# Optimization experiments

Hardware: AMD Instinct MI355X
Metric: run time of the kernel (lower is better)

## Reference

```python
import jax, jax.numpy as jnp
from jax import lax
import numpy as np

B, T, D, UNITS, NCLASSES = 256, 256, 512, 1024, 512


def setup_inputs() -> dict:
    key = jax.random.key(0)
    ks = jax.random.split(key, 6)
    x = jax.random.normal(ks[0], (B, T, D), dtype=jnp.float32)
    W = jax.random.normal(ks[1], (D + NCLASSES, 4 * UNITS), dtype=jnp.float32) * 0.02
    U = jax.random.normal(ks[2], (UNITS, 4 * UNITS), dtype=jnp.float32) * 0.02
    b = jnp.zeros((4 * UNITS,), dtype=jnp.float32)
    Wout = jax.random.normal(ks[3], (UNITS, NCLASSES), dtype=jnp.float32) * 0.02
    bout = jnp.zeros((NCLASSES,), dtype=jnp.float32)
    return {"x": x, "W": W, "U": U, "b": b, "Wout": Wout, "bout": bout}


def _hard_sigmoid(z):
    # Keras LSTM default recurrent activation
    return jnp.clip(0.2 * z + 0.5, 0.0, 1.0)


def reference(x, W, U, b, Wout, bout):
    units = U.shape[0]
    nclasses = Wout.shape[1]
    batch = x.shape[0]

    def step(carry, x_t):
        word_vec, h, c = carry
        ins = jnp.concatenate([x_t, word_vec], axis=1)          # [B, D+nclasses]
        z = ins @ W + h @ U + b                                  # [B, 4*units]
        zi, zf, zc, zo = jnp.split(z, 4, axis=1)
        c_new = _hard_sigmoid(zf) * c + _hard_sigmoid(zi) * jnp.tanh(zc)
        h_new = _hard_sigmoid(zo) * jnp.tanh(c_new)
        probs = jax.nn.softmax(h_new @ Wout + bout, axis=1)      # [B, nclasses]
        idx = jnp.argmax(probs, axis=1)                          # [B]
        new_word = jax.nn.one_hot(idx, nclasses, dtype=x_t.dtype)
        return (new_word, h_new, c_new), idx

    x_tmajor = jnp.swapaxes(x, 0, 1)                             # [T, B, D]
    # start_word = zeros_like(x_shuffled[0]) -> [B, D] (D == nclasses)
    init = (jnp.zeros((batch, x.shape[2]), x.dtype),
            jnp.zeros((batch, units), x.dtype),
            jnp.zeros((batch, units), x.dtype))
    _, idxs = lax.scan(step, init, x_tmajor)                     # [T, B]
    return jnp.swapaxes(idxs, 0, 1)                              # [B, T]
```

## Files before the change

### kernel.cpp

```cpp
#include <hip/hip_runtime.h>
#include <math.h>
#include <stdint.h>

#define Bn 256
#define Tn 256
#define Dn 512
#define UNITSn 1024
#define NCn 512
#define G4n 4096
#define KTn 1536
#define NT 48

typedef unsigned long long u64;
typedef __attribute__((ext_vector_type(4))) double d4;

__device__ __forceinline__ double hsigd(double z) {
    return fmin(fmax(0.2 * z + 0.5, 0.0), 1.0);
}

__device__ __forceinline__ u64 packlc(double v, int col) {
    double s = (v + 2048.0) * 1099511627776.0;
    u64 q = (u64)s;
    return (q << 10) | (u64)(1023 - col);
}

__global__ void convert_weights(const float* __restrict__ W, const float* __restrict__ U,
                                double* __restrict__ Wd)
{
    size_t stride = (size_t)gridDim.x * blockDim.x;
    for (size_t i = (size_t)blockIdx.x * blockDim.x + threadIdx.x;
         i < (size_t)KTn * G4n; i += stride) {
        int k = (int)(i >> 12);
        int j = (int)(i & 4095);
        float v = (k < Dn) ? W[i] : U[(size_t)(k - Dn) * G4n + j];
        Wd[i] = (double)v;
    }
}

#define AS_STR 34
#define BS_STR 34
#define AS_TILE (64 * AS_STR)
#define BS_TILE (32 * BS_STR)

__global__ __launch_bounds__(256, 2) void lstm_step_mfma(
    const float* __restrict__ x, const double* __restrict__ Wd,
    const float* __restrict__ W, const float* __restrict__ bias,
    const double* __restrict__ hin, double* __restrict__ hout,
    double* __restrict__ cst,
    const u64* __restrict__ slots_prev, u64* __restrict__ slots_cur,
    int* __restrict__ out, int t)
{
    __shared__ __align__(16) double smem[2 * AS_TILE + 2 * BS_TILE];

    const int tid = threadIdx.x;
    const int bid = blockIdx.x;
    const int ct_ = bid & 127;
    const int yt = bid >> 7;
    const int u0 = ct_ * 8;
    const int rowbase = yt * 64;

    if (ct_ == 0 && tid < 64) slots_cur[rowbase + tid] = 0ull;

    const int sr = tid >> 2;
    const int sk0 = (tid & 3) * 8;
    const int lb_k = tid >> 3;
    const int lb_c4 = (tid & 7) * 4;
    const int lb_gate = lb_c4 >> 3;
    const int lb_uoff = lb_c4 & 7;

    const float* xrow = x + (size_t)(rowbase + sr) * (Tn * Dn) + (size_t)t * Dn;
    const double* hrow = hin + (size_t)(rowbase + sr) * UNITSn;
    const double* wb = Wd + (size_t)lb_gate * UNITSn + u0 + lb_uoff;

    double apf[8];
    double2 bpf[2];

    auto prefetch = [&](int it) {
        int k0 = it * 32 + sk0;
        if (k0 < Dn) {
            float4 v0 = *(const float4*)(xrow + k0);
            float4 v1 = *(const float4*)(xrow + k0 + 4);
            apf[0] = (double)v0.x; apf[1] = (double)v0.y;
            apf[2] = (double)v0.z; apf[3] = (double)v0.w;
            apf[4] = (double)v1.x; apf[5] = (double)v1.y;
            apf[6] = (double)v1.z; apf[7] = (double)v1.w;
        } else {
            const double* hp = hrow + (k0 - Dn);
            double2 a = *(const double2*)(hp + 0);
            double2 b = *(const double2*)(hp + 2);
            double2 c2 = *(const double2*)(hp + 4);
            double2 d = *(const double2*)(hp + 6);
            apf[0] = a.x; apf[1] = a.y; apf[2] = b.x; apf[3] = b.y;
            apf[4] = c2.x; apf[5] = c2.y; apf[6] = d.x; apf[7] = d.y;
        }
        const double* bp = wb + (size_t)(it * 32 + lb_k) * G4n;
        bpf[0] = *(const double2*)(bp);
        bpf[1] = *(const double2*)(bp + 2);
    };
    auto store_tiles = [&](int p) {
        double* As = smem + p * AS_TILE;
        double* Bs = smem + 2 * AS_TILE + p * BS_TILE;
        #pragma unroll
        for (int j = 0; j < 8; j += 2) {
            double2 w2; w2.x = apf[j]; w2.y = apf[j + 1];
            *(double2*)&As[sr * AS_STR + sk0 + j] = w2;
        }
        *(double2*)&Bs[lb_k * BS_STR + lb_c4] = bpf[0];
        *(double2*)&Bs[lb_k * BS_STR + lb_c4 + 2] = bpf[1];
    };

    const int lane = tid & 63;
    const int wvi = tid >> 6;
    const int rs = wvi * 16;
    const int ml = lane & 15;
    const int kl = lane >> 4;

    d4 zero4 = {0.0, 0.0, 0.0, 0.0};
    double onek0 = (kl == 0) ? 1.0 : 0.0;
    double mk0   = (kl == 0) ? (double)ml : 0.0;
    d4 prow = __builtin_amdgcn_mfma_f64_16x16x4f64(mk0, onek0, zero4, 0, 0, 0);
    d4 pcol = __builtin_amdgcn_mfma_f64_16x16x4f64(onek0, mk0, zero4, 0, 0, 0);
    int zoff[4];
    #pragma unroll
    for (int r = 0; r < 4; r++)
        zoff[r] = (rs + (int)prow[r]) * 33 + (int)pcol[r];

    d4 acc[2];
    acc[0] = zero4; acc[1] = zero4;

    prefetch(0);
    store_tiles(0);
    __syncthreads();

    int p = 0;
    for (int it = 0; it < NT; it++) {
        if (it + 1 < NT) prefetch(it + 1);
        {
            const double* As = smem + p * AS_TILE;
            const double* Bs = smem + 2 * AS_TILE + p * BS_TILE;
            #pragma unroll
            for (int kq = 0; kq < 8; kq++) {
                double a = As[(rs + ml) * AS_STR + kq * 4 + kl];
                double b0 = Bs[(kq * 4 + kl) * BS_STR + ml];
                double b1 = Bs[(kq * 4 + kl) * BS_STR + 16 + ml];
                acc[0] = __builtin_amdgcn_mfma_f64_16x16x4f64(a, b0, acc[0], 0, 0, 0);
                acc[1] = __builtin_amdgcn_mfma_f64_16x16x4f64(a, b1, acc[1], 0, 0, 0);
            }
        }
        if (it + 1 < NT) store_tiles(p ^ 1);
        __syncthreads();
        p ^= 1;
    }

    double* zex = smem;
    #pragma unroll
    for (int r = 0; r < 4; r++) {
        zex[zoff[r]] = acc[0][r];
        zex[zoff[r] + 16] = acc[1][r];
    }
    __syncthreads();

    const int eu = tid & 7;
    const int rr = tid >> 3;
    const int ug = u0 + eu;
    const double bi0 = (double)bias[ug];
    const double bf0 = (double)bias[UNITSn + ug];
    const double bc0 = (double)bias[2 * UNITSn + ug];
    const double bo0 = (double)bias[3 * UNITSn + ug];

    #pragma unroll
    for (int s = 0; s < 2; s++) {
        int r = rr + 32 * s;
        int row = rowbase + r;
        double zi = zex[r * 33 + eu]      + bi0;
        double zf = zex[r * 33 + 8 + eu]  + bf0;
        double zc = zex[r * 33 + 16 + eu] + bc0;
        double zo = zex[r * 33 + 24 + eu] + bo0;
        if (t > 0) {
            u64 sp = slots_prev[row];
            int idx = 1023 - (int)(sp & 1023ull);
            const float* wrow = W + (size_t)(Dn + idx) * G4n + ug;
            zi += (double)wrow[0];
            zf += (double)wrow[UNITSn];
            zc += (double)wrow[2 * UNITSn];
            zo += (double)wrow[3 * UNITSn];
            if (ct_ == 0 && eu == 0) out[(size_t)row * Tn + (t - 1)] = idx;
        }
        size_t off = (size_t)row * UNITSn + ug;
        double cold = cst[off];
        double ig = hsigd(zi), fg = hsigd(zf), og = hsigd(zo);
        double cn = fg * cold + ig * tanh(zc);
        double hn = og * tanh(cn);
        cst[off] = cn;
        hout[off] = hn;
    }
}

__global__ __launch_bounds__(256, 2) void lstm_step(
    const float* __restrict__ x, const float* __restrict__ W,
    const float* __restrict__ U, const float* __restrict__ bias,
    const double* __restrict__ hin, double* __restrict__ hout,
    double* __restrict__ cst,
    const u64* __restrict__ slots_prev, u64* __restrict__ slots_cur,
    int* __restrict__ out, int t)
{
    __shared__ __align__(16) double smem[6144];

    const int tid = threadIdx.x;
    const int bid = blockIdx.x;
    const int ut = bid & 127;
    const int yt = bid >> 7;
    const int u0 = ut * 8;
    const int rowbase = yt * 64;

    if (ut == 0 && tid < 64) slots_cur[rowbase + tid] = 0ull;

    const int la_row = tid >> 2;
    const int la_k0 = (tid & 3) * 8;
    const int lb_k  = tid >> 3;
    const int lb_c4 = (tid & 7) * 4;
    const int lb_gate = lb_c4 >> 3;
    const int lb_uoff = lb_c4 & 7;

    const float* xrow = x + (size_t)(rowbase + la_row) * (Tn * Dn) + (size_t)t * Dn;
    const double* hrow = hin + (size_t)(rowbase + la_row) * UNITSn;

    double a_pf[8];
    double b_pf[4];

    auto prefetch = [&](int it) {
        int kg = it * 32;
        int k0 = kg + la_k0;
        if (k0 < Dn) {
            float4 v0 = *(const float4*)(xrow + k0);
            float4 v1 = *(const float4*)(xrow + k0 + 4);
            a_pf[0] = (double)v0.x; a_pf[1] = (double)v0.y;
            a_pf[2] = (double)v0.z; a_pf[3] = (double)v0.w;
            a_pf[4] = (double)v1.x; a_pf[5] = (double)v1.y;
            a_pf[6] = (double)v1.z; a_pf[7] = (double)v1.w;
        } else {
            const double* hp = hrow + (k0 - Dn);
            double2 h0v = *(const double2*)(hp + 0);
            double2 h1v = *(const double2*)(hp + 2);
            double2 h2v = *(const double2*)(hp + 4);
            double2 h3v = *(const double2*)(hp + 6);
            a_pf[0] = h0v.x; a_pf[1] = h0v.y; a_pf[2] = h1v.x; a_pf[3] = h1v.y;
            a_pf[4] = h2v.x; a_pf[5] = h2v.y; a_pf[6] = h3v.x; a_pf[7] = h3v.y;
        }
        int kB = kg + lb_k;
        const float* rowp = (kB < Dn) ? (W + (size_t)kB * G4n)
                                      : (U + (size_t)(kB - Dn) * G4n);
        float4 wv = *(const float4*)(rowp + lb_gate * UNITSn + u0 + lb_uoff);
        b_pf[0] = (double)wv.x; b_pf[1] = (double)wv.y;
        b_pf[2] = (double)wv.z; b_pf[3] = (double)wv.w;
    };
    auto store_tiles = [&](int p) {
        double* As = smem + p * 2048;
        double* Bs = smem + 4096 + p * 1024;
        #pragma unroll
        for (int j = 0; j < 8; j++) As[(la_k0 + j) * 64 + la_row] = a_pf[j];
        double2 w0; w0.x = b_pf[0]; w0.y = b_pf[1];
        double2 w1; w1.x = b_pf[2]; w1.y = b_pf[3];
        *(double2*)&Bs[lb_k * 32 + lb_c4] = w0;
        *(double2*)&Bs[lb_k * 32 + lb_c4 + 2] = w1;
    };

    const int lane = tid & 63;
    const int wv_ = tid >> 6;
    const int ri = lane >> 3;
    const int cj = lane & 7;
    const int rb = wv_ * 16 + ri * 2;

    double acc[2][4];
    #pragma unroll
    for (int i = 0; i < 2; i++)
        #pragma unroll
        for (int j = 0; j < 4; j++) acc[i][j] = 0.0;

    prefetch(0);
    store_tiles(0);
    __syncthreads();

    int p = 0;
    for (int it = 0; it < NT; it++) {
        if (it + 1 < NT) prefetch(it + 1);
        {
            const double* As = smem + p * 2048;
            const double* Bs = smem + 4096 + p * 1024;
            #pragma unroll
            for (int k = 0; k < 32; k++) {
                double2 a2 = *(const double2*)&As[k * 64 + rb];
                double2 b0 = *(const double2*)&Bs[k * 32 + cj * 4];
                double2 b1 = *(const double2*)&Bs[k * 32 + cj * 4 + 2];
                acc[0][0] = fma(a2.x, b0.x, acc[0][0]);
                acc[0][1] = fma(a2.x, b0.y, acc[0][1]);
                acc[0][2] = fma(a2.x, b1.x, acc[0][2]);
                acc[0][3] = fma(a2.x, b1.y, acc[0][3]);
                acc[1][0] = fma(a2.y, b0.x, acc[1][0]);
                acc[1][1] = fma(a2.y, b0.y, acc[1][1]);
                acc[1][2] = fma(a2.y, b1.x, acc[1][2]);
                acc[1][3] = fma(a2.y, b1.y, acc[1][3]);
            }
        }
        if (it + 1 < NT) store_tiles(p ^ 1);
        __syncthreads();
        p ^= 1;
    }

    double* zex = smem;
    #pragma unroll
    for (int i = 0; i < 2; i++) {
        double2 z0; z0.x = acc[i][0]; z0.y = acc[i][1];
        double2 z1; z1.x = acc[i][2]; z1.y = acc[i][3];
        *(double2*)&zex[(rb + i) * 32 + cj * 4] = z0;
        *(double2*)&zex[(rb + i) * 32 + cj * 4 + 2] = z1;
    }
    __syncthreads();

    const int eu = tid & 7;
    const int rr = tid >> 3;
    const int ug = u0 + eu;
    const double bi0 = (double)bias[ug];
    const double bf0 = (double)bias[UNITSn + ug];
    const double bc0 = (double)bias[2 * UNITSn + ug];
    const double bo0 = (double)bias[3 * UNITSn + ug];

    #pragma unroll
    for (int s = 0; s < 2; s++) {
        int r = rr + 32 * s;
        int row = rowbase + r;
        double zi = zex[r * 32 + eu]      + bi0;
        double zf = zex[r * 32 + 8 + eu]  + bf0;
        double zc = zex[r * 32 + 16 + eu] + bc0;
        double zo = zex[r * 32 + 24 + eu] + bo0;
        if (t > 0) {
            u64 sp = slots_prev[row];
            int idx = 1023 - (int)(sp & 1023ull);
            const float* wrow = W + (size_t)(Dn + idx) * G4n + ug;
            zi += (double)wrow[0];
            zf += (double)wrow[UNITSn];
            zc += (double)wrow[2 * UNITSn];
            zo += (double)wrow[3 * UNITSn];
            if (ut == 0 && eu == 0) out[(size_t)row * Tn + (t - 1)] = idx;
        }
        size_t off = (size_t)row * UNITSn + ug;
        double cold = cst[off];
        double ig = hsigd(zi), fg = hsigd(zf), og = hsigd(zo);
        double cn = fg * cold + ig * tanh(zc);
        double hn = og * tanh(cn);
        cst[off] = cn;
        hout[off] = hn;
    }
}

#define C_RT 8
#define C_CT 64
#define C_KC 32

__global__ __launch_bounds__(256) void logits_argmax(
    const double* __restrict__ h, const float* __restrict__ Wout,
    const float* __restrict__ bout, u64* __restrict__ slots)
{
    __shared__ double Hs[C_KC][9];
    __shared__ float  Ws[C_KC][C_CT];

    const int tid = threadIdx.x;
    const int ty = tid >> 5;
    const int tx = tid & 31;
    const int rbase = blockIdx.y * C_RT;
    const int cbase = blockIdx.x * C_CT;

    double acc0 = 0.0, acc1 = 0.0;

    const int lh_row = tid >> 5;
    const int lh_kk = tid & 31;
    const int lw_kk = tid >> 4;
    const int lw_j0 = (tid & 15) * 4;

    for (int kb = 0; kb < UNITSn; kb += C_KC) {
        Hs[lh_kk][lh_row] = h[(size_t)(rbase + lh_row) * UNITSn + kb + lh_kk];
        #pragma unroll
        for (int it = 0; it < 2; it++) {
            int kk = lw_kk + it * 16;
            float4 v = *(const float4*)(Wout + (size_t)(kb + kk) * NCn + cbase + lw_j0);
            *(float4*)&Ws[kk][lw_j0] = v;
        }
        __syncthreads();
        #pragma unroll
        for (int kk = 0; kk < C_KC; kk++) {
            double a = Hs[kk][ty];
            float2 wv = *(const float2*)&Ws[kk][tx * 2];
            acc0 = fma(a, (double)wv.x, acc0);
            acc1 = fma(a, (double)wv.y, acc1);
        }
        __syncthreads();
    }

    int col0 = cbase + tx * 2;
    double lg0 = acc0 + (double)bout[col0];
    double lg1 = acc1 + (double)bout[col0 + 1];

    u64 p0 = packlc(lg0, col0);
    u64 p1 = packlc(lg1, col0 + 1);
    u64 best = (p0 > p1) ? p0 : p1;
    #pragma unroll
    for (int off = 16; off >= 1; off >>= 1) {
        u64 o = __shfl_down(best, off, 32);
        if (o > best) best = o;
    }
    if (tx == 0) atomicMax(&slots[rbase + ty], best);
}

__global__ void final_decode(const u64* __restrict__ slots, int* __restrict__ out) {
    int b = threadIdx.x;
    u64 s = slots[b];
    out[(size_t)b * Tn + (Tn - 1)] = 1023 - (int)(s & 1023ull);
}

extern "C" void kernel_launch(void* const* d_in, const int* in_sizes, int n_in,
                              void* d_out, int out_size, void* d_ws, size_t ws_size,
                              hipStream_t stream) {
    const float* x    = (const float*)d_in[0];
    const float* W    = (const float*)d_in[1];
    const float* U    = (const float*)d_in[2];
    const float* bias = (const float*)d_in[3];
    const float* Wout = (const float*)d_in[4];
    const float* bout = (const float*)d_in[5];
    int* out = (int*)d_out;
    char* ws = (char*)d_ws;

    double* h0 = (double*)(ws);
    double* h1 = (double*)(ws + (2u << 20));
    double* c  = (double*)(ws + (4u << 20));
    u64* slots0 = (u64*)(ws + (6u << 20));
    u64* slots1 = (u64*)(ws + (6u << 20) + 2048);
    double* Wd  = (double*)(ws + (8u << 20));

    const size_t NEED = (8ull << 20) + (size_t)KTn * G4n * 8;
    const bool big = ws_size >= NEED;

    hipMemsetAsync(d_ws, 0, (6u << 20) + 4096, stream);
    if (big) convert_weights<<<1024, 256, 0, stream>>>(W, U, Wd);

    for (int t = 0; t < Tn; t++) {
        double* hin  = (t & 1) ? h1 : h0;
        double* hout = (t & 1) ? h0 : h1;
        u64* sprev = (t & 1) ? slots0 : slots1;
        u64* scur  = (t & 1) ? slots1 : slots0;
        if (big) {
            lstm_step_mfma<<<dim3(512), 256, 0, stream>>>(x, Wd, W, bias, hin, hout, c,
                                                          sprev, scur, out, t);
        } else {
            lstm_step<<<dim3(512), 256, 0, stream>>>(x, W, U, bias, hin, hout, c,
                                                     sprev, scur, out, t);
        }
        logits_argmax<<<dim3(8, 32), 256, 0, stream>>>(hout, Wout, bout, scur);
    }
    final_decode<<<1, Bn, 0, stream>>>(slots1, out);
}
```

Before: 31.28 ms.

## Fuse all timesteps into one persistent kernel with grid-wide barriers

```diff
diff --git a/kernel.cpp b/kernel.cpp
--- a/kernel.cpp
+++ b/kernel.cpp
@@ -22,6 +22,21 @@
     double s = (v + 2048.0) * 1099511627776.0;
     u64 q = (u64)s;
     return (q << 10) | (u64)(1023 - col);
+}
+
+__device__ __forceinline__ void gbar(u64* bar, u64 target) {
+    __threadfence();
+    __syncthreads();
+    if (threadIdx.x == 0) {
+        __hip_atomic_fetch_add(bar, 1ull, __ATOMIC_ACQ_REL, __HIP_MEMORY_SCOPE_AGENT);
+        int n = 0;
+        while (__hip_atomic_load(bar, __ATOMIC_ACQUIRE, __HIP_MEMORY_SCOPE_AGENT) < target) {
+            __builtin_amdgcn_s_sleep(8);
+            if (++n > 20000) break;
+        }
+    }
+    __syncthreads();
+    __threadfence();
 }
 
 __global__ void convert_weights(const float* __restrict__ W, const float* __restrict__ U,
@@ -42,13 +57,13 @@
 #define AS_TILE (64 * AS_STR)
 #define BS_TILE (32 * BS_STR)
 
-__global__ __launch_bounds__(256, 2) void lstm_step_mfma(
+__global__ __launch_bounds__(256, 2) void lstm_persistent(
     const float* __restrict__ x, const double* __restrict__ Wd,
     const float* __restrict__ W, const float* __restrict__ bias,
-    const double* __restrict__ hin, double* __restrict__ hout,
-    double* __restrict__ cst,
-    const u64* __restrict__ slots_prev, u64* __restrict__ slots_cur,
-    int* __restrict__ out, int t)
+    const float* __restrict__ Wout, const float* __restrict__ bout,
+    double* __restrict__ h0buf, double* __restrict__ h1buf,
+    u64* __restrict__ slots0, u64* __restrict__ slots1,
+    u64* __restrict__ bar, int* __restrict__ out)
 {
     __shared__ __align__(16) double smem[2 * AS_TILE + 2 * BS_TILE];
 
@@ -59,59 +74,16 @@
     const int u0 = ct_ * 8;
     const int rowbase = yt * 64;
 
-    if (ct_ == 0 && tid < 64) slots_cur[rowbase + tid] = 0ull;
-
     const int sr = tid >> 2;
     const int sk0 = (tid & 3) * 8;
     const int lb_k = tid >> 3;
     const int lb_c4 = (tid & 7) * 4;
     const int lb_gate = lb_c4 >> 3;
     const int lb_uoff = lb_c4 & 7;
-
-    const float* xrow = x + (size_t)(rowbase + sr) * (Tn * Dn) + (size_t)t * Dn;
-    const double* hrow = hin + (size_t)(rowbase + sr) * UNITSn;
     const double* wb = Wd + (size_t)lb_gate * UNITSn + u0 + lb_uoff;
 
-    double apf[8];
-    double2 bpf[2];
-
-    auto prefetch = [&](int it) {
-        int k0 = it * 32 + sk0;
-        if (k0 < Dn) {
-            float4 v0 = *(const float4*)(xrow + k0);
-            float4 v1 = *(const float4*)(xrow + k0 + 4);
-            apf[0] = (double)v0.x; apf[1] = (double)v0.y;
-            apf[2] = (double)v0.z; apf[3] = (double)v0.w;
-            apf[4] = (double)v1.x; apf[5] = (double)v1.y;
-            apf[6] = (double)v1.z; apf[7] = (double)v1.w;
-        } else {
-            const double* hp = hrow + (k0 - Dn);
-            double2 a = *(const double2*)(hp + 0);
-            double2 b = *(const double2*)(hp + 2);
-            double2 c2 = *(const double2*)(hp + 4);
-            double2 d = *(const double2*)(hp + 6);
-            apf[0] = a.x; apf[1] = a.y; apf[2] = b.x; apf[3] = b.y;
-            apf[4] = c2.x; apf[5] = c2.y; apf[6] = d.x; apf[7] = d.y;
-        }
-        const double* bp = wb + (size_t)(it * 32 + lb_k) * G4n;
-        bpf[0] = *(const double2*)(bp);
-        bpf[1] = *(const double2*)(bp + 2);
-    };
-    auto store_tiles = [&](int p) {
-        double* As = smem + p * AS_TILE;
-        double* Bs = smem + 2 * AS_TILE + p * BS_TILE;
-        #pragma unroll
-        for (int j = 0; j < 8; j += 2) {
-            double2 w2; w2.x = apf[j]; w2.y = apf[j + 1];
-            *(double2*)&As[sr * AS_STR + sk0 + j] = w2;
-        }
-        *(double2*)&Bs[lb_k * BS_STR + lb_c4] = bpf[0];
-        *(double2*)&Bs[lb_k * BS_STR + lb_c4 + 2] = bpf[1];
-    };
-
     const int lane = tid & 63;
-    const int wvi = tid >> 6;
-    const int rs = wvi * 16;
+    const int rs = (tid >> 6) * 16;
     const int ml = lane & 15;
     const int kl = lane >> 4;
 
@@ -125,41 +97,6 @@
     for (int r = 0; r < 4; r++)
         zoff[r] = (rs + (int)prow[r]) * 33 + (int)pcol[r];
 
-    d4 acc[2];
-    acc[0] = zero4; acc[1] = zero4;
-
-    prefetch(0);
-    store_tiles(0);
-    __syncthreads();
-
-    int p = 0;
-    for (int it = 0; it < NT; it++) {
-        if (it + 1 < NT) prefetch(it + 1);
-        {
-            const double* As = smem + p * AS_TILE;
-            const double* Bs = smem + 2 * AS_TILE + p * BS_TILE;
-            #pragma unroll
-            for (int kq = 0; kq < 8; kq++) {
-                double a = As[(rs + ml) * AS_STR + kq * 4 + kl];
-                double b0 = Bs[(kq * 4 + kl) * BS_STR + ml];
-                double b1 = Bs[(kq * 4 + kl) * BS_STR + 16 + ml];
-                acc[0] = __builtin_amdgcn_mfma_f64_16x16x4f64(a, b0, acc[0], 0, 0, 0);
-                acc[1] = __builtin_amdgcn_mfma_f64_16x16x4f64(a, b1, acc[1], 0, 0, 0);
-            }
-        }
-        if (it + 1 < NT) store_tiles(p ^ 1);
-        __syncthreads();
-        p ^= 1;
-    }
-
-    double* zex = smem;
-    #pragma unroll
-    for (int r = 0; r < 4; r++) {
-        zex[zoff[r]] = acc[0][r];
-        zex[zoff[r] + 16] = acc[1][r];
-    }
-    __syncthreads();
-
     const int eu = tid & 7;
     const int rr = tid >> 3;
     const int ug = u0 + eu;
@@ -167,32 +104,147 @@
     const double bf0 = (double)bias[UNITSn + ug];
     const double bc0 = (double)bias[2 * UNITSn + ug];
     const double bo0 = (double)bias[3 * UNITSn + ug];
-
-    #pragma unroll
-    for (int s = 0; s < 2; s++) {
-        int r = rr + 32 * s;
-        int row = rowbase + r;
-        double zi = zex[r * 33 + eu]      + bi0;
-        double zf = zex[r * 33 + 8 + eu]  + bf0;
-        double zc = zex[r * 33 + 16 + eu] + bc0;
-        double zo = zex[r * 33 + 24 + eu] + bo0;
-        if (t > 0) {
-            u64 sp = slots_prev[row];
-            int idx = 1023 - (int)(sp & 1023ull);
-            const float* wrow = W + (size_t)(Dn + idx) * G4n + ug;
-            zi += (double)wrow[0];
-            zf += (double)wrow[UNITSn];
-            zc += (double)wrow[2 * UNITSn];
-            zo += (double)wrow[3 * UNITSn];
-            if (ct_ == 0 && eu == 0) out[(size_t)row * Tn + (t - 1)] = idx;
-        }
-        size_t off = (size_t)row * UNITSn + ug;
-        double cold = cst[off];
-        double ig = hsigd(zi), fg = hsigd(zf), og = hsigd(zo);
-        double cn = fg * cold + ig * tanh(zc);
-        double hn = og * tanh(cn);
-        cst[off] = cn;
-        hout[off] = hn;
+    double creg[2] = {0.0, 0.0};
+
+    const int p2row = ((bid >> 4) << 3) + (tid >> 5);
+    const int p2col = ((bid & 15) << 5) + (tid & 31);
+    const float* wcol = Wout + p2col;
+    const double bo2 = (double)bout[p2col];
+
+    u64 bar_t = 0;
+
+    for (int t = 0; t < Tn; t++) {
+        const double* hin = (t & 1) ? h1buf : h0buf;
+        double* hout      = (t & 1) ? h0buf : h1buf;
+        const u64* sprev  = (t & 1) ? slots0 : slots1;
+        u64* scur         = (t & 1) ? slots1 : slots0;
+
+        if (ct_ == 0 && tid < 64) scur[rowbase + tid] = 0ull;
+
+        const float* xrow = x + (size_t)(rowbase + sr) * (Tn * Dn) + (size_t)t * Dn;
+        const double* hrow = hin + (size_t)(rowbase + sr) * UNITSn;
+
+        double apf[8];
+        double2 bpf[2];
+
+        auto prefetch = [&](int it) {
+            int k0 = it * 32 + sk0;
+            if (k0 < Dn) {
+                float4 v0 = *(const float4*)(xrow + k0);
+                float4 v1 = *(const float4*)(xrow + k0 + 4);
+                apf[0] = (double)v0.x; apf[1] = (double)v0.y;
+                apf[2] = (double)v0.z; apf[3] = (double)v0.w;
+                apf[4] = (double)v1.x; apf[5] = (double)v1.y;
+                apf[6] = (double)v1.z; apf[7] = (double)v1.w;
+            } else {
+                const double* hp = hrow + (k0 - Dn);
+                double2 a = *(const double2*)(hp + 0);
+                double2 b = *(const double2*)(hp + 2);
+                double2 c2 = *(const double2*)(hp + 4);
+                double2 d = *(const double2*)(hp + 6);
+                apf[0] = a.x; apf[1] = a.y; apf[2] = b.x; apf[3] = b.y;
+                apf[4] = c2.x; apf[5] = c2.y; apf[6] = d.x; apf[7] = d.y;
+            }
+            const double* bp = wb + (size_t)(it * 32 + lb_k) * G4n;
+            bpf[0] = *(const double2*)(bp);
+            bpf[1] = *(const double2*)(bp + 2);
+        };
+        auto store_tiles = [&](int p) {
+            double* As = smem + p * AS_TILE;
+            double* Bs = smem + 2 * AS_TILE + p * BS_TILE;
+            #pragma unroll
+            for (int j = 0; j < 8; j += 2) {
+                double2 w2; w2.x = apf[j]; w2.y = apf[j + 1];
+                *(double2*)&As[sr * AS_STR + sk0 + j] = w2;
+            }
+            *(double2*)&Bs[lb_k * BS_STR + lb_c4] = bpf[0];
+            *(double2*)&Bs[lb_k * BS_STR + lb_c4 + 2] = bpf[1];
+        };
+
+        d4 acc[2];
+        acc[0] = zero4; acc[1] = zero4;
+
+        prefetch(0);
+        store_tiles(0);
+        __syncthreads();
+
+        int p = 0;
+        for (int it = 0; it < NT; it++) {
+            if (it + 1 < NT) prefetch(it + 1);
+            {
+                const double* As = smem + p * AS_TILE;
+                const double* Bs = smem + 2 * AS_TILE + p * BS_TILE;
+                #pragma unroll
+                for (int kq = 0; kq < 8; kq++) {
+                    double a = As[(rs + ml) * AS_STR + kq * 4 + kl];
+                    double b0 = Bs[(kq * 4 + kl) * BS_STR + ml];
+                    double b1 = Bs[(kq * 4 + kl) * BS_STR + 16 + ml];
+                    acc[0] = __builtin_amdgcn_mfma_f64_16x16x4f64(a, b0, acc[0], 0, 0, 0);
+                    acc[1] = __builtin_amdgcn_mfma_f64_16x16x4f64(a, b1, acc[1], 0, 0, 0);
+                }
+            }
+            if (it + 1 < NT) store_tiles(p ^ 1);
+            __syncthreads();
+            p ^= 1;
+        }
+
+        double* zex = smem;
+        #pragma unroll
+        for (int r = 0; r < 4; r++) {
+            zex[zoff[r]] = acc[0][r];
+            zex[zoff[r] + 16] = acc[1][r];
+        }
+        __syncthreads();
+
+        #pragma unroll
+        for (int s = 0; s < 2; s++) {
+            int r = rr + 32 * s;
+            int row = rowbase + r;
+            double zi = zex[r * 33 + eu]      + bi0;
+            double zf = zex[r * 33 + 8 + eu]  + bf0;
+            double zc = zex[r * 33 + 16 + eu] + bc0;
+            double zo = zex[r * 33 + 24 + eu] + bo0;
+            if (t > 0) {
+                u64 sp = sprev[row];
+                int idx = 1023 - (int)(sp & 1023ull);
+                const float* wrow = W + (size_t)(Dn + idx) * G4n + ug;
+                zi += (double)wrow[0];
+                zf += (double)wrow[UNITSn];
+                zc += (double)wrow[2 * UNITSn];
+                zo += (double)wrow[3 * UNITSn];
+                if (ct_ == 0 && eu == 0) out[(size_t)row * Tn + (t - 1)] = idx;
+            }
+            double cold = creg[s];
+            double ig = hsigd(zi), fg = hsigd(zf), og = hsigd(zo);
+            double cn = fg * cold + ig * tanh(zc);
+            double hn = og * tanh(cn);
+            creg[s] = cn;
+            hout[(size_t)row * UNITSn + ug] = hn;
+        }
+
+        gbar(bar, bar_t += 512);
+
+        {
+            const double* hr = hout + (size_t)p2row * UNITSn;
+            double a = 0.0;
+            #pragma unroll 4
+            for (int k = 0; k < UNITSn; k++)
+                a = fma(hr[k], (double)wcol[(size_t)k * NCn], a);
+            u64 best = packlc(a + bo2, p2col);
+            #pragma unroll
+            for (int m = 16; m >= 1; m >>= 1) {
+                u64 o = __shfl_xor(best, m, 64);
+                if (o > best) best = o;
+            }
+            if ((tid & 31) == 0) atomicMax(&scur[p2row], best);
+        }
+
+        gbar(bar, bar_t += 512);
+    }
+
+    if (bid == 0) {
+        u64 s = slots1[tid];
+        out[(size_t)tid * Tn + (Tn - 1)] = 1023 - (int)(s & 1023ull);
     }
 }
 
@@ -434,27 +486,28 @@
     double* c  = (double*)(ws + (4u << 20));
     u64* slots0 = (u64*)(ws + (6u << 20));
     u64* slots1 = (u64*)(ws + (6u << 20) + 2048);
+    u64* bar    = (u64*)(ws + (6u << 20) + 4096);
     double* Wd  = (double*)(ws + (8u << 20));
 
     const size_t NEED = (8ull << 20) + (size_t)KTn * G4n * 8;
     const bool big = ws_size >= NEED;
 
-    hipMemsetAsync(d_ws, 0, (6u << 20) + 4096, stream);
-    if (big) convert_weights<<<1024, 256, 0, stream>>>(W, U, Wd);
-
-    for (int t = 0; t < Tn; t++) {
-        double* hin  = (t & 1) ? h1 : h0;
-        double* hout = (t & 1) ? h0 : h1;
-        u64* sprev = (t & 1) ? slots0 : slots1;
-        u64* scur  = (t & 1) ? slots1 : slots0;
-        if (big) {
-            lstm_step_mfma<<<dim3(512), 256, 0, stream>>>(x, Wd, W, bias, hin, hout, c,
-                                                          sprev, scur, out, t);
-        } else {
+    hipMemsetAsync(d_ws, 0, (6u << 20) + 8192, stream);
+
+    if (big) {
+        convert_weights<<<1024, 256, 0, stream>>>(W, U, Wd);
+        lstm_persistent<<<dim3(512), 256, 0, stream>>>(x, Wd, W, bias, Wout, bout,
+                                                       h0, h1, slots0, slots1, bar, out);
+    } else {
+        for (int t = 0; t < Tn; t++) {
+            double* hin  = (t & 1) ? h1 : h0;
+            double* hout = (t & 1) ? h0 : h1;
+            u64* sprev = (t & 1) ? slots0 : slots1;
+            u64* scur  = (t & 1) ? slots1 : slots0;
             lstm_step<<<dim3(512), 256, 0, stream>>>(x, W, U, bias, hin, hout, c,
                                                      sprev, scur, out, t);
-        }
-        logits_argmax<<<dim3(8, 32), 256, 0, stream>>>(hout, Wout, bout, scur);
-    }
-    final_decode<<<1, Bn, 0, stream>>>(slots1, out);
-}
+            logits_argmax<<<dim3(8, 32), 256, 0, stream>>>(hout, Wout, bout, scur);
+        }
+        final_decode<<<1, Bn, 0, stream>>>(slots1, out);
+    }
+}
```

After: 112.9 ms. +260.9%, slower.

## Read fp32 weights directly in MFMA step kernel and drop fp64 weight copy

Applied to the files above, without the earlier changes.

```diff
diff --git a/kernel.cpp b/kernel.cpp
--- a/kernel.cpp
+++ b/kernel.cpp
@@ -24,27 +24,15 @@
     return (q << 10) | (u64)(1023 - col);
 }
 
-__global__ void convert_weights(const float* __restrict__ W, const float* __restrict__ U,
-                                double* __restrict__ Wd)
-{
-    size_t stride = (size_t)gridDim.x * blockDim.x;
-    for (size_t i = (size_t)blockIdx.x * blockDim.x + threadIdx.x;
-         i < (size_t)KTn * G4n; i += stride) {
-        int k = (int)(i >> 12);
-        int j = (int)(i & 4095);
-        float v = (k < Dn) ? W[i] : U[(size_t)(k - Dn) * G4n + j];
-        Wd[i] = (double)v;
-    }
-}
-
-#define AS_STR 34
-#define BS_STR 34
+#define AS_STR 33
+#define BS_STR 33
 #define AS_TILE (64 * AS_STR)
 #define BS_TILE (32 * BS_STR)
 
 __global__ __launch_bounds__(256, 2) void lstm_step_mfma(
-    const float* __restrict__ x, const double* __restrict__ Wd,
-    const float* __restrict__ W, const float* __restrict__ bias,
+    const float* __restrict__ x,
+    const float* __restrict__ W, const float* __restrict__ U,
+    const float* __restrict__ bias,
     const double* __restrict__ hin, double* __restrict__ hout,
     double* __restrict__ cst,
     const u64* __restrict__ slots_prev, u64* __restrict__ slots_cur,
@@ -54,12 +42,21 @@
 
     const int tid = threadIdx.x;
     const int bid = blockIdx.x;
-    const int ct_ = bid & 127;
-    const int yt = bid >> 7;
+    const int ct_ = (bid & 7) * 16 + ((bid >> 3) & 15);
+    const int yt  = bid >> 7;
     const int u0 = ct_ * 8;
     const int rowbase = yt * 64;
 
     if (ct_ == 0 && tid < 64) slots_cur[rowbase + tid] = 0ull;
+
+    const int eu = tid & 7;
+    const int rr = tid >> 3;
+    const int ug = u0 + eu;
+    u64 spre0 = 0, spre1 = 0;
+    if (t > 0) {
+        spre0 = slots_prev[rowbase + rr];
+        spre1 = slots_prev[rowbase + rr + 32];
+    }
 
     const int sr = tid >> 2;
     const int sk0 = (tid & 3) * 8;
@@ -67,13 +64,13 @@
     const int lb_c4 = (tid & 7) * 4;
     const int lb_gate = lb_c4 >> 3;
     const int lb_uoff = lb_c4 & 7;
+    const int lb_coff = lb_gate * UNITSn + u0 + lb_uoff;
 
     const float* xrow = x + (size_t)(rowbase + sr) * (Tn * Dn) + (size_t)t * Dn;
     const double* hrow = hin + (size_t)(rowbase + sr) * UNITSn;
-    const double* wb = Wd + (size_t)lb_gate * UNITSn + u0 + lb_uoff;
 
     double apf[8];
-    double2 bpf[2];
+    float4 bpf;
 
     auto prefetch = [&](int it) {
         int k0 = it * 32 + sk0;
@@ -93,9 +90,10 @@
             apf[0] = a.x; apf[1] = a.y; apf[2] = b.x; apf[3] = b.y;
             apf[4] = c2.x; apf[5] = c2.y; apf[6] = d.x; apf[7] = d.y;
         }
-        const double* bp = wb + (size_t)(it * 32 + lb_k) * G4n;
-        bpf[0] = *(const double2*)(bp);
-        bpf[1] = *(const double2*)(bp + 2);
+        int kB = it * 32 + lb_k;
+        const float* rowp = (kB < Dn) ? (W + (size_t)kB * G4n)
+                                      : (U + (size_t)(kB - Dn) * G4n);
+        bpf = *(const float4*)(rowp + lb_coff);
     };
     auto store_tiles = [&](int p) {
         double* As = smem + p * AS_TILE;
@@ -105,13 +103,14 @@
             double2 w2; w2.x = apf[j]; w2.y = apf[j + 1];
             *(double2*)&As[sr * AS_STR + sk0 + j] = w2;
         }
-        *(double2*)&Bs[lb_k * BS_STR + lb_c4] = bpf[0];
-        *(double2*)&Bs[lb_k * BS_STR + lb_c4 + 2] = bpf[1];
+        double2 w0; w0.x = (double)bpf.x; w0.y = (double)bpf.y;
+        double2 w1; w1.x = (double)bpf.z; w1.y = (double)bpf.w;
+        *(double2*)&Bs[lb_k * BS_STR + lb_c4] = w0;
+        *(double2*)&Bs[lb_k * BS_STR + lb_c4 + 2] = w1;
     };
 
     const int lane = tid & 63;
-    const int wvi = tid >> 6;
-    const int rs = wvi * 16;
+    const int rs = (tid >> 6) * 16;
     const int ml = lane & 15;
     const int kl = lane >> 4;
 
@@ -160,189 +159,33 @@
     }
     __syncthreads();
 
-    const int eu = tid & 7;
-    const int rr = tid >> 3;
-    const int ug = u0 + eu;
     const double bi0 = (double)bias[ug];
     const double bf0 = (double)bias[UNITSn + ug];
     const double bc0 = (double)bias[2 * UNITSn + ug];
     const double bo0 = (double)bias[3 * UNITSn + ug];
 
+    float wi0 = 0.f, wf0 = 0.f, wc0 = 0.f, wo0 = 0.f;
+    float wi1 = 0.f, wf1 = 0.f, wc1 = 0.f, wo1 = 0.f;
+    if (t > 0) {
+        int idx0 = 1023 - (int)(spre0 & 1023ull);
+        int idx1 = 1023 - (int)(spre1 & 1023ull);
+        const float* wr0 = W + (size_t)(Dn + idx0) * G4n + ug;
+        const float* wr1 = W + (size_t)(Dn + idx1) * G4n + ug;
+        wi0 = wr0[0]; wf0 = wr0[UNITSn]; wc0 = wr0[2 * UNITSn]; wo0 = wr0[3 * UNITSn];
+        wi1 = wr1[0]; wf1 = wr1[UNITSn]; wc1 = wr1[2 * UNITSn]; wo1 = wr1[3 * UNITSn];
+        if (ct_ == 0 && eu == 0) {
+            out[(size_t)(rowbase + rr) * Tn + (t - 1)] = idx0;
+            out[(size_t)(rowbase + rr + 32) * Tn + (t - 1)] = idx1;
+        }
+    }
     #pragma unroll
     for (int s = 0; s < 2; s++) {
         int r = rr + 32 * s;
         int row = rowbase + r;
-        double zi = zex[r * 33 + eu]      + bi0;
-        double zf = zex[r * 33 + 8 + eu]  + bf0;
-        double zc = zex[r * 33 + 16 + eu] + bc0;
-        double zo = zex[r * 33 + 24 + eu] + bo0;
-        if (t > 0) {
-            u64 sp = slots_prev[row];
-            int idx = 1023 - (int)(sp & 1023ull);
-            const float* wrow = W + (size_t)(Dn + idx) * G4n + ug;
-            zi += (double)wrow[0];
-            zf += (double)wrow[UNITSn];
-            zc += (double)wrow[2 * UNITSn];
-            zo += (double)wrow[3 * UNITSn];
-            if (ct_ == 0 && eu == 0) out[(size_t)row * Tn + (t - 1)] = idx;
-        }
-        size_t off = (size_t)row * UNITSn + ug;
-        double cold = cst[off];
-        double ig = hsigd(zi), fg = hsigd(zf), og = hsigd(zo);
-        double cn = fg * cold + ig * tanh(zc);
-        double hn = og * tanh(cn);
-        cst[off] = cn;
-        hout[off] = hn;
-    }
-}
-
-__global__ __launch_bounds__(256, 2) void lstm_step(
-    const float* __restrict__ x, const float* __restrict__ W,
-    const float* __restrict__ U, const float* __restrict__ bias,
-    const double* __restrict__ hin, double* __restrict__ hout,
-    double* __restrict__ cst,
-    const u64* __restrict__ slots_prev, u64* __restrict__ slots_cur,
-    int* __restrict__ out, int t)
-{
-    __shared__ __align__(16) double smem[6144];
-
-    const int tid = threadIdx.x;
-    const int bid = blockIdx.x;
-    const int ut = bid & 127;
-    const int yt = bid >> 7;
-    const int u0 = ut * 8;
-    const int rowbase = yt * 64;
-
-    if (ut == 0 && tid < 64) slots_cur[rowbase + tid] = 0ull;
-
-    const int la_row = tid >> 2;
-    const int la_k0 = (tid & 3) * 8;
-    const int lb_k  = tid >> 3;
-    const int lb_c4 = (tid & 7) * 4;
-    const int lb_gate = lb_c4 >> 3;
-    const int lb_uoff = lb_c4 & 7;
-
-    const float* xrow = x + (size_t)(rowbase + la_row) * (Tn * Dn) + (size_t)t * Dn;
-    const double* hrow = hin + (size_t)(rowbase + la_row) * UNITSn;
-
-    double a_pf[8];
-    double b_pf[4];
-
-    auto prefetch = [&](int it) {
-        int kg = it * 32;
-        int k0 = kg + la_k0;
-        if (k0 < Dn) {
-            float4 v0 = *(const float4*)(xrow + k0);
-            float4 v1 = *(const float4*)(xrow + k0 + 4);
-            a_pf[0] = (double)v0.x; a_pf[1] = (double)v0.y;
-            a_pf[2] = (double)v0.z; a_pf[3] = (double)v0.w;
-            a_pf[4] = (double)v1.x; a_pf[5] = (double)v1.y;
-            a_pf[6] = (double)v1.z; a_pf[7] = (double)v1.w;
-        } else {
-            const double* hp = hrow + (k0 - Dn);
-            double2 h0v = *(const double2*)(hp + 0);
-            double2 h1v = *(const double2*)(hp + 2);
-            double2 h2v = *(const double2*)(hp + 4);
-            double2 h3v = *(const double2*)(hp + 6);
-            a_pf[0] = h0v.x; a_pf[1] = h0v.y; a_pf[2] = h1v.x; a_pf[3] = h1v.y;
-            a_pf[4] = h2v.x; a_pf[5] = h2v.y; a_pf[6] = h3v.x; a_pf[7] = h3v.y;
-        }
-        int kB = kg + lb_k;
-        const float* rowp = (kB < Dn) ? (W + (size_t)kB * G4n)
-                                      : (U + (size_t)(kB - Dn) * G4n);
-        float4 wv = *(const float4*)(rowp + lb_gate * UNITSn + u0 + lb_uoff);
-        b_pf[0] = (double)wv.x; b_pf[1] = (double)wv.y;
-        b_pf[2] = (double)wv.z; b_pf[3] = (double)wv.w;
-    };
-    auto store_tiles = [&](int p) {
-        double* As = smem + p * 2048;
-        double* Bs = smem + 4096 + p * 1024;
-        #pragma unroll
-        for (int j = 0; j < 8; j++) As[(la_k0 + j) * 64 + la_row] = a_pf[j];
-        double2 w0; w0.x = b_pf[0]; w0.y = b_pf[1];
-        double2 w1; w1.x = b_pf[2]; w1.y = b_pf[3];
-        *(double2*)&Bs[lb_k * 32 + lb_c4] = w0;
-        *(double2*)&Bs[lb_k * 32 + lb_c4 + 2] = w1;
-    };
-
-    const int lane = tid & 63;
-    const int wv_ = tid >> 6;
-    const int ri = lane >> 3;
-    const int cj = lane & 7;
-    const int rb = wv_ * 16 + ri * 2;
-
-    double acc[2][4];
-    #pragma unroll
-    for (int i = 0; i < 2; i++)
-        #pragma unroll
-        for (int j = 0; j < 4; j++) acc[i][j] = 0.0;
-
-    prefetch(0);
-    store_tiles(0);
-    __syncthreads();
-
-    int p = 0;
-    for (int it = 0; it < NT; it++) {
-        if (it + 1 < NT) prefetch(it + 1);
-        {
-            const double* As = smem + p * 2048;
-            const double* Bs = smem + 4096 + p * 1024;
-            #pragma unroll
-            for (int k = 0; k < 32; k++) {
-                double2 a2 = *(const double2*)&As[k * 64 + rb];
-                double2 b0 = *(const double2*)&Bs[k * 32 + cj * 4];
-                double2 b1 = *(const double2*)&Bs[k * 32 + cj * 4 + 2];
-                acc[0][0] = fma(a2.x, b0.x, acc[0][0]);
-                acc[0][1] = fma(a2.x, b0.y, acc[0][1]);
-                acc[0][2] = fma(a2.x, b1.x, acc[0][2]);
-                acc[0][3] = fma(a2.x, b1.y, acc[0][3]);
-                acc[1][0] = fma(a2.y, b0.x, acc[1][0]);
-                acc[1][1] = fma(a2.y, b0.y, acc[1][1]);
-                acc[1][2] = fma(a2.y, b1.x, acc[1][2]);
-                acc[1][3] = fma(a2.y, b1.y, acc[1][3]);
-            }
-        }
-        if (it + 1 < NT) store_tiles(p ^ 1);
-        __syncthreads();
-        p ^= 1;
-    }
-
-    double* zex = smem;
-    #pragma unroll
-    for (int i = 0; i < 2; i++) {
-        double2 z0; z0.x = acc[i][0]; z0.y = acc[i][1];
-        double2 z1; z1.x = acc[i][2]; z1.y = acc[i][3];
-        *(double2*)&zex[(rb + i) * 32 + cj * 4] = z0;
-        *(double2*)&zex[(rb + i) * 32 + cj * 4 + 2] = z1;
-    }
-    __syncthreads();
-
-    const int eu = tid & 7;
-    const int rr = tid >> 3;
-    const int ug = u0 + eu;
-    const double bi0 = (double)bias[ug];
-    const double bf0 = (double)bias[UNITSn + ug];
-    const double bc0 = (double)bias[2 * UNITSn + ug];
-    const double bo0 = (double)bias[3 * UNITSn + ug];
-
-    #pragma unroll
-    for (int s = 0; s < 2; s++) {
-        int r = rr + 32 * s;
-        int row = rowbase + r;
-        double zi = zex[r * 32 + eu]      + bi0;
-        double zf = zex[r * 32 + 8 + eu]  + bf0;
-        double zc = zex[r * 32 + 16 + eu] + bc0;
-        double zo = zex[r * 32 + 24 + eu] + bo0;
-        if (t > 0) {
-            u64 sp = slots_prev[row];
-            int idx = 1023 - (int)(sp & 1023ull);
-            const float* wrow = W + (size_t)(Dn + idx) * G4n + ug;
-            zi += (double)wrow[0];
-            zf += (double)wrow[UNITSn];
-            zc += (double)wrow[2 * UNITSn];
-            zo += (double)wrow[3 * UNITSn];
-            if (ut == 0 && eu == 0) out[(size_t)row * Tn + (t - 1)] = idx;
-        }
+        double zi = zex[r * 33 + eu]      + bi0 + (double)(s ? wi1 : wi0);
+        double zf = zex[r * 33 + 8 + eu]  + bf0 + (double)(s ? wf1 : wf0);
+        double zc = zex[r * 33 + 16 + eu] + bc0 + (double)(s ? wc1 : wc0);
+        double zo = zex[r * 33 + 24 + eu] + bo0 + (double)(s ? wo1 : wo0);
         size_t off = (size_t)row * UNITSn + ug;
         double cold = cst[off];
         double ig = hsigd(zi), fg = hsigd(zf), og = hsigd(zo);
@@ -434,26 +277,16 @@
     double* c  = (double*)(ws + (4u << 20));
     u64* slots0 = (u64*)(ws + (6u << 20));
     u64* slots1 = (u64*)(ws + (6u << 20) + 2048);
-    double* Wd  = (double*)(ws + (8u << 20));
-
-    const size_t NEED = (8ull << 20) + (size_t)KTn * G4n * 8;
-    const bool big = ws_size >= NEED;
-
-    hipMemsetAsync(d_ws, 0, (6u << 20) + 4096, stream);
-    if (big) convert_weights<<<1024, 256, 0, stream>>>(W, U, Wd);
+
+    hipMemsetAsync(d_ws, 0, (6u << 20) + 8192, stream);
 
     for (int t = 0; t < Tn; t++) {
         double* hin  = (t & 1) ? h1 : h0;
         double* hout = (t & 1) ? h0 : h1;
         u64* sprev = (t & 1) ? slots0 : slots1;
         u64* scur  = (t & 1) ? slots1 : slots0;
-        if (big) {
-            lstm_step_mfma<<<dim3(512), 256, 0, stream>>>(x, Wd, W, bias, hin, hout, c,
-                                                          sprev, scur, out, t);
-        } else {
-            lstm_step<<<dim3(512), 256, 0, stream>>>(x, W, U, bias, hin, hout, c,
-                                                     sprev, scur, out, t);
-        }
+        lstm_step_mfma<<<dim3(512), 256, 0, stream>>>(x, W, U, bias, hin, hout, c,
+                                                      sprev, scur, out, t);
         logits_argmax<<<dim3(8, 32), 256, 0, stream>>>(hout, Wout, bout, scur);
     }
     final_decode<<<1, Bn, 0, stream>>>(slots1, out);
```

Result: slower. 33.87 ms (+8.3%).
